# Optimization experiments

Measured on AMD Instinct MI355X. Metric: run time of the kernel, lower is better.

## Reference

```python
import jax, jax.numpy as jnp
import numpy as np

N = 50000
T = 6
E = 800000
F_IN = 64
HID = 64
HEADS = 4
NEG_SLOPE = 0.2
BN_EPS = 1e-5


def _gat_layer(x, src, dst, W, att_src, att_dst, bias, concat):
    # x: [N, Fin]; W: [Fin, H*C]; att_*: [H, C]; src/dst: [E+N] (self loops appended)
    n = x.shape[0]
    H, C = att_src.shape
    xl = (x @ W).reshape(n, H, C)                     # [N, H, C]
    a_src = jnp.sum(xl * att_src[None], axis=-1)      # [N, H]
    a_dst = jnp.sum(xl * att_dst[None], axis=-1)      # [N, H]
    e = jax.nn.leaky_relu(a_src[src] + a_dst[dst], NEG_SLOPE)  # [E', H]
    # segment softmax over destination nodes (every node has a self loop)
    m = jax.ops.segment_max(e, dst, num_segments=n)
    ex = jnp.exp(e - m[dst])
    s = jax.ops.segment_sum(ex, dst, num_segments=n)
    alpha = ex / (s[dst] + 1e-16)                     # [E', H]
    msg = alpha[:, :, None] * xl[src]                 # [E', H, C]
    out = jax.ops.segment_sum(msg, dst, num_segments=n)  # [N, H, C]
    if concat:
        out = out.reshape(n, H * C)
    else:
        out = out.mean(axis=1)
    return out + bias


def _forward(x_seq, edge_index, W1, as1, ad1, b1, W2, as2, ad2, b2,
             cw1, cb1, g1, be1, cw2, cb2, g2, be2, lw1, lb1, lw2, lb2):
    n = x_seq.shape[1]
    self_loop = jnp.arange(n, dtype=edge_index.dtype)
    src = jnp.concatenate([edge_index[0], self_loop])
    dst = jnp.concatenate([edge_index[1], self_loop])

    def per_t(x):
        h = _gat_layer(x, src, dst, W1, as1, ad1, b1, concat=True)
        h = jax.nn.elu(h)
        h = _gat_layer(h, src, dst, W2, as2, ad2, b2, concat=False)
        h = jax.nn.elu(h)
        return h                                      # [N, HID]

    temporal = jax.vmap(per_t)(x_seq)                 # [T, N, HID]
    temporal = jnp.transpose(temporal, (1, 2, 0))     # [N, HID, T]

    def conv_bn_relu(t, cw, cb, g, be):
        y = jax.lax.conv_general_dilated(
            t, cw, window_strides=(1,), padding=[(1, 1)],
            dimension_numbers=('NCH', 'OIH', 'NCH')) + cb[None, :, None]
        # BatchNorm1d in eval mode, running_mean=0, running_var=1
        y = y * (g / jnp.sqrt(1.0 + BN_EPS))[None, :, None] + be[None, :, None]
        return jax.nn.relu(y)

    t = conv_bn_relu(temporal, cw1, cb1, g1, be1)
    t = conv_bn_relu(t, cw2, cb2, g2, be2)
    pooled = t.mean(axis=-1)                          # adaptive avg pool -> [N, HID]
    h = jax.nn.relu(pooled @ lw1 + lb1)
    logits = h @ lw2 + lb2                            # [N, 1]
    return logits


def setup_inputs() -> dict:
    key = jax.random.key(0)
    ks = jax.random.split(key, 20)
    C1 = HID // HEADS  # 16
    s = 0.1
    return {
        'x_seq': jax.random.normal(ks[0], (T, N, F_IN), jnp.float32),
        'edge_index': jax.random.randint(ks[1], (2, E), 0, N, jnp.int32),
        'W1': jax.random.normal(ks[2], (F_IN, HEADS * C1), jnp.float32) * s,
        'as1': jax.random.normal(ks[3], (HEADS, C1), jnp.float32) * s,
        'ad1': jax.random.normal(ks[4], (HEADS, C1), jnp.float32) * s,
        'b1': jnp.zeros((HEADS * C1,), jnp.float32),
        'W2': jax.random.normal(ks[5], (HID, HEADS * HID), jnp.float32) * s,
        'as2': jax.random.normal(ks[6], (HEADS, HID), jnp.float32) * s,
        'ad2': jax.random.normal(ks[7], (HEADS, HID), jnp.float32) * s,
        'b2': jnp.zeros((HID,), jnp.float32),
        'cw1': jax.random.normal(ks[8], (HID, HID, 3), jnp.float32) * s,
        'cb1': jnp.zeros((HID,), jnp.float32),
        'g1': jnp.ones((HID,), jnp.float32),
        'be1': jnp.zeros((HID,), jnp.float32),
        'cw2': jax.random.normal(ks[9], (HID, HID, 3), jnp.float32) * s,
        'cb2': jnp.zeros((HID,), jnp.float32),
        'g2': jnp.ones((HID,), jnp.float32),
        'be2': jnp.zeros((HID,), jnp.float32),
        'lw1': jax.random.normal(ks[10], (HID, HID // 2), jnp.float32) * s,
        'lb1': jnp.zeros((HID // 2,), jnp.float32),
        'lw2': jax.random.normal(ks[11], (HID // 2, 1), jnp.float32) * s,
        'lb2': jnp.zeros((1,), jnp.float32),
    }


def reference(x_seq, edge_index, W1, as1, ad1, b1, W2, as2, ad2, b2,
              cw1, cb1, g1, be1, cw2, cb2, g2, be2, lw1, lb1, lw2, lb2):
    return _forward(x_seq, edge_index, W1, as1, ad1, b1, W2, as2, ad2, b2,
                    cw1, cb1, g1, be1, cw2, cb2, g2, be2, lw1, lb1, lw2, lb2)
```

## Files before the change

kernel.cpp:

```cpp
#include <hip/hip_runtime.h>
#include <math.h>

#define NN 50000
#define EE 800000
#define TT 6

__device__ __forceinline__ float lrelu(float x){ return x > 0.f ? x : 0.2f*x; }
__device__ __forceinline__ float eluf(float x){ return x > 0.f ? x : expm1f(x); }
#define RL(v,i) __uint_as_float(__builtin_amdgcn_readlane(__float_as_uint(v), (i)))

__global__ void k_init_counts(int* __restrict__ c){
  int i = blockIdx.x*256 + threadIdx.x;
  if (i < NN) c[i] = 1;
}

__global__ void k_hist(const int* __restrict__ dst, int* __restrict__ c){
  int i = blockIdx.x*256 + threadIdx.x;
  if (i < EE) atomicAdd(&c[dst[i]], 1);
}

__global__ void k_scanA(const int* __restrict__ cnt, int* __restrict__ excl,
                        int* __restrict__ bsum){
  __shared__ int sh[1024];
  int tid = threadIdx.x;
  int i = blockIdx.x*1024 + tid;
  int v = (i < NN) ? cnt[i] : 0;
  int x = v;
  sh[tid] = x; __syncthreads();
  for (int off = 1; off < 1024; off <<= 1){
    int y = (tid >= off) ? sh[tid - off] : 0;
    __syncthreads();
    x += y; sh[tid] = x; __syncthreads();
  }
  if (i < NN) excl[i] = x - v;
  if (tid == 1023) bsum[blockIdx.x] = x;
}

__global__ void k_scanB(int* __restrict__ bsum, int nb){
  if (threadIdx.x == 0){
    int run = 0;
    for (int b = 0; b < nb; ++b){ int t = bsum[b]; bsum[b] = run; run += t; }
  }
}

__global__ void k_scanC(const int* __restrict__ excl, const int* __restrict__ bsum,
                        int* __restrict__ rowptr, int* __restrict__ cursor){
  int i = blockIdx.x*1024 + threadIdx.x;
  if (i < NN){
    int v = excl[i] + bsum[blockIdx.x];
    rowptr[i] = v; cursor[i] = v;
  }
  if (i == 0) rowptr[NN] = EE + NN;
}

__global__ void k_scatter(const int* __restrict__ ei, int* __restrict__ cursor,
                          int* __restrict__ csr){
  int i = blockIdx.x*256 + threadIdx.x;
  if (i < EE){
    int d = ei[EE + i];
    int p = atomicAdd(&cursor[d], 1);
    csr[p] = ei[i];
  } else if (i < EE + NN){
    int v = i - EE;
    int p = atomicAdd(&cursor[v], 1);
    csr[p] = v;
  }
}

__global__ void k_prep(const float* __restrict__ W1, const float* __restrict__ as1,
                       const float* __restrict__ ad1,
                       const float* __restrict__ W2, const float* __restrict__ as2,
                       const float* __restrict__ ad2,
                       const float* __restrict__ cw1, const float* __restrict__ cw2,
                       float* __restrict__ Was1, float* __restrict__ Wad1,
                       float* __restrict__ Wat2, float* __restrict__ Wb,
                       float4* __restrict__ w1p, float4* __restrict__ w2p){
  int tid = threadIdx.x;
  int k = tid >> 2, h = tid & 3;
  float s1 = 0.f, d1 = 0.f, s2 = 0.f, d2 = 0.f;
  for (int c = 0; c < 16; ++c){
    float w = W1[k*64 + h*16 + c];
    s1 += w * as1[h*16 + c];
    d1 += w * ad1[h*16 + c];
  }
  for (int c = 0; c < 64; ++c){
    float w = W2[k*256 + h*64 + c];
    s2 += w * as2[h*64 + c];
    d2 += w * ad2[h*64 + c];
  }
  Was1[k*4+h] = s1; Wad1[k*4+h] = d1;
  Wat2[k*8 + h] = s2; Wat2[k*8 + 4 + h] = d2;
  for (int idx = tid; idx < 256*64; idx += 256){
    int kf = idx >> 6, c = idx & 63;
    int hh = kf >> 6, kk = kf & 63;
    Wb[idx] = W2[kk*256 + hh*64 + c];
  }
  for (int idx = tid; idx < 64*64; idx += 256){
    int o = idx & 63, i = idx >> 6;
    w1p[idx] = make_float4(cw1[o*192+i*3], cw1[o*192+i*3+1], cw1[o*192+i*3+2], 0.f);
    w2p[idx] = make_float4(cw2[o*192+i*3], cw2[o*192+i*3+1], cw2[o*192+i*3+2], 0.f);
  }
}

__global__ __launch_bounds__(256) void k_gemm_att1(const float* __restrict__ A,
                            const float* __restrict__ W,
                            const float* __restrict__ Was, const float* __restrict__ Wad,
                            float* __restrict__ Xl, float* __restrict__ a_src,
                            float* __restrict__ a_dst){
  __shared__ float At[64][16];
  int tid = threadIdx.x;
  int r0 = blockIdx.x * 16;
  {
    const float4* A4 = (const float4*)(A + (size_t)r0*64);
    float4 v = A4[tid];
    int r = tid >> 4, k4 = (tid & 15) << 2;
    At[k4+0][r] = v.x; At[k4+1][r] = v.y;
    At[k4+2][r] = v.z; At[k4+3][r] = v.w;
  }
  __syncthreads();
  int col = tid & 63;
  int rbase = (tid >> 6) << 2;
  float acc0=0.f, acc1=0.f, acc2=0.f, acc3=0.f;
  for (int k = 0; k < 64; ++k){
    float w = W[k*64 + col];
    float4 a4 = *(const float4*)&At[k][rbase];
    acc0 += a4.x*w; acc1 += a4.y*w; acc2 += a4.z*w; acc3 += a4.w*w;
  }
  Xl[(size_t)(r0+rbase+0)*64 + col] = acc0;
  Xl[(size_t)(r0+rbase+1)*64 + col] = acc1;
  Xl[(size_t)(r0+rbase+2)*64 + col] = acc2;
  Xl[(size_t)(r0+rbase+3)*64 + col] = acc3;
  if (tid < 128){
    int r = tid >> 3, jx = tid & 7;
    int h = jx & 3;
    const float* Wv = (jx < 4) ? Was : Wad;
    float a = 0.f;
    for (int k = 0; k < 64; ++k) a += At[k][r] * Wv[k*4 + h];
    if (jx < 4) a_src[(r0 + r)*4 + h] = a;
    else        a_dst[(r0 + r)*4 + h] = a;
  }
}

__global__ __launch_bounds__(256) void k_att(const float* __restrict__ A,
                                             const float* __restrict__ Wat,
                                             float* __restrict__ a_src,
                                             float* __restrict__ a_dst){
  int lane = threadIdx.x & 63;
  int wid  = threadIdx.x >> 6;
  int q = lane >> 3, j = lane & 7;
  int n = blockIdx.x*32 + wid*8 + q;
  if (n >= NN) return;
  const float* __restrict__ Ar = A + (size_t)n*64;
  float s = 0.f;
#pragma unroll 8
  for (int k = 0; k < 64; ++k) s += Ar[k] * Wat[k*8 + j];
  if (j < 4) a_src[n*4 + j] = s;
  else       a_dst[n*4 + (j-4)] = s;
}

__global__ void k_agg1(const float* __restrict__ xl, const float* __restrict__ a_src,
                       const float* __restrict__ a_dst, const float* __restrict__ b1,
                       const int* __restrict__ rowptr, const int* __restrict__ csr,
                       float* __restrict__ h1){
  int lane = threadIdx.x & 63;
  int wid  = threadIdx.x >> 6;
  int n = blockIdx.x*4 + wid;
  int h = lane >> 4;
  float ad = a_dst[n*4 + h];
  int rs = rowptr[n], re = rowptr[n+1];
  float s = 0.f, acc = 0.f;
  int j = rs;
  for (; j + 4 <= re; j += 4){
    int sn0=csr[j], sn1=csr[j+1], sn2=csr[j+2], sn3=csr[j+3];
    float e0=a_src[sn0*4+h], e1=a_src[sn1*4+h], e2=a_src[sn2*4+h], e3=a_src[sn3*4+h];
    float x0=xl[(size_t)sn0*64+lane], x1=xl[(size_t)sn1*64+lane];
    float x2=xl[(size_t)sn2*64+lane], x3=xl[(size_t)sn3*64+lane];
    float p0=__expf(lrelu(e0+ad)), p1=__expf(lrelu(e1+ad));
    float p2=__expf(lrelu(e2+ad)), p3=__expf(lrelu(e3+ad));
    s += p0; acc += p0*x0;
    s += p1; acc += p1*x1;
    s += p2; acc += p2*x2;
    s += p3; acc += p3*x3;
  }
  for (; j < re; ++j){
    int sn = csr[j];
    float p = __expf(lrelu(a_src[sn*4+h] + ad));
    float x = xl[(size_t)sn*64 + lane];
    s += p; acc += p*x;
  }
  h1[(size_t)n*64 + lane] = eluf(acc/(s + 1e-16f) + b1[lane]);
}

__global__ void k_agg2(const float* __restrict__ h1, const float* __restrict__ a_src,
                       const float* __restrict__ a_dst,
                       const int* __restrict__ rowptr, const int* __restrict__ csr,
                       float* __restrict__ agg){
  int lane = threadIdx.x & 63;
  int wid  = threadIdx.x >> 6;
  int n = blockIdx.x*4 + wid;
  float4 ad = ((const float4*)a_dst)[n];
  int rs = rowptr[n], re = rowptr[n+1];
  float s0=0.f,s1=0.f,s2=0.f,s3=0.f;
  float g0=0.f,g1=0.f,g2=0.f,g3=0.f;
  int j = rs;
  for (; j + 4 <= re; j += 4){
    int sa=csr[j], sb=csr[j+1], sc=csr[j+2], sd=csr[j+3];
    float4 ea = ((const float4*)a_src)[sa];
    float4 eb = ((const float4*)a_src)[sb];
    float4 ec = ((const float4*)a_src)[sc];
    float4 ed = ((const float4*)a_src)[sd];
    float xa = h1[(size_t)sa*64 + lane];
    float xb = h1[(size_t)sb*64 + lane];
    float xc = h1[(size_t)sc*64 + lane];
    float xd = h1[(size_t)sd*64 + lane];
    float pa0=__expf(lrelu(ea.x+ad.x)), pa1=__expf(lrelu(ea.y+ad.y));
    float pa2=__expf(lrelu(ea.z+ad.z)), pa3=__expf(lrelu(ea.w+ad.w));
    float pb0=__expf(lrelu(eb.x+ad.x)), pb1=__expf(lrelu(eb.y+ad.y));
    float pb2=__expf(lrelu(eb.z+ad.z)), pb3=__expf(lrelu(eb.w+ad.w));
    float pc0=__expf(lrelu(ec.x+ad.x)), pc1=__expf(lrelu(ec.y+ad.y));
    float pc2=__expf(lrelu(ec.z+ad.z)), pc3=__expf(lrelu(ec.w+ad.w));
    float pd0=__expf(lrelu(ed.x+ad.x)), pd1=__expf(lrelu(ed.y+ad.y));
    float pd2=__expf(lrelu(ed.z+ad.z)), pd3=__expf(lrelu(ed.w+ad.w));
    s0 += pa0+pb0+pc0+pd0; g0 += pa0*xa + pb0*xb + pc0*xc + pd0*xd;
    s1 += pa1+pb1+pc1+pd1; g1 += pa1*xa + pb1*xb + pc1*xc + pd1*xd;
    s2 += pa2+pb2+pc2+pd2; g2 += pa2*xa + pb2*xb + pc2*xc + pd2*xd;
    s3 += pa3+pb3+pc3+pd3; g3 += pa3*xa + pb3*xb + pc3*xc + pd3*xd;
  }
  for (; j < re; ++j){
    int sn = csr[j];
    float4 ev = ((const float4*)a_src)[sn];
    float x = h1[(size_t)sn*64 + lane];
    float p0=__expf(lrelu(ev.x+ad.x)), p1=__expf(lrelu(ev.y+ad.y));
    float p2=__expf(lrelu(ev.z+ad.z)), p3=__expf(lrelu(ev.w+ad.w));
    s0 += p0; g0 += p0*x;
    s1 += p1; g1 += p1*x;
    s2 += p2; g2 += p2*x;
    s3 += p3; g3 += p3*x;
  }
  size_t base = (size_t)n*256 + lane;
  agg[base      ] = g0/(s0 + 1e-16f);
  agg[base +  64] = g1/(s1 + 1e-16f);
  agg[base + 128] = g2/(s2 + 1e-16f);
  agg[base + 192] = g3/(s3 + 1e-16f);
}

__global__ __launch_bounds__(256) void k_out2(const float* __restrict__ agg,
                                              const float* __restrict__ Wb,
                                              const float* __restrict__ b2,
                                              float* __restrict__ ht){
  int lane = threadIdx.x & 63;
  int wid  = __builtin_amdgcn_readfirstlane(threadIdx.x >> 6);
  int r0 = blockIdx.x*16 + wid*4;
  const float* __restrict__ a0 = agg + (size_t)r0*256;
  float acc0=0.f, acc1=0.f, acc2=0.f, acc3=0.f;
#pragma unroll 4
  for (int k = 0; k < 256; ++k){
    float w = Wb[k*64 + lane];
    acc0 += a0[k      ]*w;
    acc1 += a0[k + 256]*w;
    acc2 += a0[k + 512]*w;
    acc3 += a0[k + 768]*w;
  }
  float bb = b2[lane];
  ht[(size_t)(r0+0)*64 + lane] = eluf(0.25f*acc0 + bb);
  ht[(size_t)(r0+1)*64 + lane] = eluf(0.25f*acc1 + bb);
  ht[(size_t)(r0+2)*64 + lane] = eluf(0.25f*acc2 + bb);
  ht[(size_t)(r0+3)*64 + lane] = eluf(0.25f*acc3 + bb);
}

__global__ __launch_bounds__(256) void k_xpose(const float* __restrict__ htb,
                                               float* __restrict__ Xp){
  int ch = threadIdx.x & 63;
  int q  = threadIdx.x >> 6;
  int n = blockIdx.x*4 + q;
  float r0 = htb[((size_t)0*NN + n)*64 + ch];
  float r1 = htb[((size_t)1*NN + n)*64 + ch];
  float r2 = htb[((size_t)2*NN + n)*64 + ch];
  float r3 = htb[((size_t)3*NN + n)*64 + ch];
  float r4 = htb[((size_t)4*NN + n)*64 + ch];
  float r5 = htb[((size_t)5*NN + n)*64 + ch];
  float* dst = Xp + (size_t)n*384 + ch*6;
  *(float2*)(dst+0) = make_float2(r0,r1);
  *(float2*)(dst+2) = make_float2(r2,r3);
  *(float2*)(dst+4) = make_float2(r4,r5);
}

__global__ __launch_bounds__(256) void k_temporal(
    float* __restrict__ Xp,
    const float4* __restrict__ w1p, const float* __restrict__ cb1,
    const float* __restrict__ g1,   const float* __restrict__ be1,
    const float4* __restrict__ w2p, const float* __restrict__ cb2,
    const float* __restrict__ g2,   const float* __restrict__ be2,
    const float* __restrict__ lw1,  const float* __restrict__ lb1,
    const float* __restrict__ lw2,  const float* __restrict__ lb2,
    float* __restrict__ out){
  int lane = threadIdx.x & 63;
  int wid  = __builtin_amdgcn_readfirstlane(threadIdx.x >> 6);
  int n0 = (blockIdx.x*4 + wid)*4;
  float* xb = Xp + (size_t)n0*384;

  float acc[4][6];
  {
    float c = cb1[lane];
#pragma unroll
    for (int q=0;q<4;++q){
#pragma unroll
      for (int t=0;t<6;++t) acc[q][t]=c;
    }
    for (int i = 0; i < 64; ++i){
      float4 w = w1p[(i<<6) + lane];
      const float* xr = xb + i*6;
#pragma unroll
      for (int q = 0; q < 4; ++q){
        float2 A2 = *(const float2*)(xr + q*384);
        float2 B2 = *(const float2*)(xr + q*384 + 2);
        float2 C2 = *(const float2*)(xr + q*384 + 4);
        acc[q][0] += w.y*A2.x + w.z*A2.y;
        acc[q][1] += w.x*A2.x + w.y*A2.y + w.z*B2.x;
        acc[q][2] += w.x*A2.y + w.y*B2.x + w.z*B2.y;
        acc[q][3] += w.x*B2.x + w.y*B2.y + w.z*C2.x;
        acc[q][4] += w.x*B2.y + w.y*C2.x + w.z*C2.y;
        acc[q][5] += w.x*C2.x + w.y*C2.y;
      }
    }
    float bns = g1[lane]*rsqrtf(1.f + 1e-5f), be = be1[lane];
#pragma unroll
    for (int q=0;q<4;++q){
      float* dp = xb + q*384 + lane*6;
      float r0 = fmaxf(acc[q][0]*bns + be, 0.f);
      float r1 = fmaxf(acc[q][1]*bns + be, 0.f);
      float r2 = fmaxf(acc[q][2]*bns + be, 0.f);
      float r3 = fmaxf(acc[q][3]*bns + be, 0.f);
      float r4 = fmaxf(acc[q][4]*bns + be, 0.f);
      float r5 = fmaxf(acc[q][5]*bns + be, 0.f);
      *(float2*)(dp+0) = make_float2(r0,r1);
      *(float2*)(dp+2) = make_float2(r2,r3);
      *(float2*)(dp+4) = make_float2(r4,r5);
    }
  }
  float p0, p1, p2, p3;
  {
    float c = cb2[lane];
#pragma unroll
    for (int q=0;q<4;++q){
#pragma unroll
      for (int t=0;t<6;++t) acc[q][t]=c;
    }
    for (int i = 0; i < 64; ++i){
      float4 w = w2p[(i<<6) + lane];
      const float* xr = xb + i*6;
#pragma unroll
      for (int q = 0; q < 4; ++q){
        float2 A2 = *(const float2*)(xr + q*384);
        float2 B2 = *(const float2*)(xr + q*384 + 2);
        float2 C2 = *(const float2*)(xr + q*384 + 4);
        acc[q][0] += w.y*A2.x + w.z*A2.y;
        acc[q][1] += w.x*A2.x + w.y*A2.y + w.z*B2.x;
        acc[q][2] += w.x*A2.y + w.y*B2.x + w.z*B2.y;
        acc[q][3] += w.x*B2.x + w.y*B2.y + w.z*C2.x;
        acc[q][4] += w.x*B2.y + w.y*C2.x + w.z*C2.y;
        acc[q][5] += w.x*C2.x + w.y*C2.y;
      }
    }
    float bns = g2[lane]*rsqrtf(1.f + 1e-5f), be = be2[lane];
    float pl[4];
#pragma unroll
    for (int q=0;q<4;++q){
      float s = 0.f;
#pragma unroll
      for (int t=0;t<6;++t) s += fmaxf(acc[q][t]*bns + be, 0.f);
      pl[q] = s*(1.f/6.f);
    }
    p0 = pl[0]; p1 = pl[1]; p2 = pl[2]; p3 = pl[3];
  }
  {
    int j = lane & 31;
    float lb = lb1[j], w2v = lw2[j];
    float h0=0.f, h1v=0.f, h2=0.f, h3=0.f;
    for (int k = 0; k < 64; ++k){
      float lw = lw1[k*32 + j];
      h0  += RL(p0, k)*lw;
      h1v += RL(p1, k)*lw;
      h2  += RL(p2, k)*lw;
      h3  += RL(p3, k)*lw;
    }
    float o0 = fmaxf(h0 +lb, 0.f)*w2v;
    float o1 = fmaxf(h1v+lb, 0.f)*w2v;
    float o2 = fmaxf(h2 +lb, 0.f)*w2v;
    float o3 = fmaxf(h3 +lb, 0.f)*w2v;
#pragma unroll
    for (int off = 16; off >= 1; off >>= 1){
      o0 += __shfl_xor(o0, off);
      o1 += __shfl_xor(o1, off);
      o2 += __shfl_xor(o2, off);
      o3 += __shfl_xor(o3, off);
    }
    if (lane == 0){
      float b = lb2[0];
      out[n0+0] = o0 + b;
      out[n0+1] = o1 + b;
      out[n0+2] = o2 + b;
      out[n0+3] = o3 + b;
    }
  }
}

extern "C" void kernel_launch(void* const* d_in, const int* in_sizes, int n_in,
                              void* d_out, int out_size, void* d_ws, size_t ws_size,
                              hipStream_t stream) {
  const float* x_seq = (const float*)d_in[0];
  const int*   ei    = (const int*)  d_in[1];
  const float* W1  = (const float*)d_in[2];
  const float* as1 = (const float*)d_in[3];
  const float* ad1 = (const float*)d_in[4];
  const float* b1  = (const float*)d_in[5];
  const float* W2  = (const float*)d_in[6];
  const float* as2 = (const float*)d_in[7];
  const float* ad2 = (const float*)d_in[8];
  const float* b2  = (const float*)d_in[9];
  const float* cw1 = (const float*)d_in[10];
  const float* cb1 = (const float*)d_in[11];
  const float* g1  = (const float*)d_in[12];
  const float* be1 = (const float*)d_in[13];
  const float* cw2 = (const float*)d_in[14];
  const float* cb2 = (const float*)d_in[15];
  const float* g2  = (const float*)d_in[16];
  const float* be2 = (const float*)d_in[17];
  const float* lw1 = (const float*)d_in[18];
  const float* lb1 = (const float*)d_in[19];
  const float* lw2 = (const float*)d_in[20];
  const float* lb2 = (const float*)d_in[21];
  float* out = (float*)d_out;

  char* wp = (char*)d_ws;
  auto alloc = [&](size_t bytes) -> char* {
    char* p = wp; wp += (bytes + 255) & ~(size_t)255; return p;
  };
  float* htb  = (float*)alloc((size_t)TT*NN*64*sizeof(float));
  float* Was1 = (float*)alloc(256*sizeof(float));
  float* Wad1 = (float*)alloc(256*sizeof(float));
  float* Wat2 = (float*)alloc(64*8*sizeof(float));
  float* Wb   = (float*)alloc(256*64*sizeof(float));
  float4* w1p = (float4*)alloc(64*64*sizeof(float4));
  float4* w2p = (float4*)alloc(64*64*sizeof(float4));
  char* scratch0 = wp;
  int*   counts = (int*)  alloc(NN*sizeof(int));
  int*   excl   = (int*)  alloc(NN*sizeof(int));
  int*   bsum   = (int*)  alloc(64*sizeof(int));
  int*   rowptr = (int*)  alloc((NN+1)*sizeof(int));
  int*   cursor = (int*)  alloc(NN*sizeof(int));
  int*   csr    = (int*)  alloc((size_t)(EE+NN)*sizeof(int));
  float* a_src  = (float*)alloc((size_t)NN*4*sizeof(float));
  float* a_dst  = (float*)alloc((size_t)NN*4*sizeof(float));
  float* h1     = (float*)alloc((size_t)NN*64*sizeof(float));
  float* agg    = (float*)alloc((size_t)NN*256*sizeof(float));
  float* xl1    = agg;
  float* Xp     = (float*)scratch0;

  const int NBSCAN = (NN + 1023)/1024;
  k_init_counts<<<(NN+255)/256, 256, 0, stream>>>(counts);
  k_hist<<<(EE+255)/256, 256, 0, stream>>>(ei + EE, counts);
  k_scanA<<<NBSCAN, 1024, 0, stream>>>(counts, excl, bsum);
  k_scanB<<<1, 64, 0, stream>>>(bsum, NBSCAN);
  k_scanC<<<NBSCAN, 1024, 0, stream>>>(excl, bsum, rowptr, cursor);
  k_scatter<<<(EE+NN+255)/256, 256, 0, stream>>>(ei, cursor, csr);
  k_prep<<<1, 256, 0, stream>>>(W1, as1, ad1, W2, as2, ad2, cw1, cw2,
                                Was1, Wad1, Wat2, Wb, w1p, w2p);

  for (int t = 0; t < TT; ++t){
    const float* xt = x_seq + (size_t)t*NN*64;
    k_gemm_att1<<<NN/16, 256, 0, stream>>>(xt, W1, Was1, Wad1, xl1, a_src, a_dst);
    k_agg1<<<NN/4, 256, 0, stream>>>(xl1, a_src, a_dst, b1, rowptr, csr, h1);
    k_att<<<(NN+31)/32, 256, 0, stream>>>(h1, Wat2, a_src, a_dst);
    k_agg2<<<NN/4, 256, 0, stream>>>(h1, a_src, a_dst, rowptr, csr, agg);
    k_out2<<<NN/16, 256, 0, stream>>>(agg, Wb, b2, htb + (size_t)t*NN*64);
  }
  k_xpose<<<NN/4, 256, 0, stream>>>(htb, Xp);
  k_temporal<<<NN/16, 256, 0, stream>>>(Xp, w1p, cb1, g1, be1, w2p, cb2, g2, be2,
                                        lw1, lb1, lw2, lb2, out);
}
```

Before: 1.623 ms.

## Fuse layer-2 attention into agg1, tile out2 via LDS, restructure temporal conv

The layer-2 attention projection (the separate k_att kernel) is folded into k_agg1 through a wave shuffle reduction, which removes one launch and one re-read of h1 per timestep. k_out2 now stages the aggregated rows transposed in shared memory and reads them from LDS instead of issuing scalar global loads. The temporal stage moves to a channel-major, zero-padded layout with one node per lane, spread across two kernels (transpose, then fused conv1+conv2+pool+MLP), so weights become wave-uniform and activation loads are coalesced. The cost is an extra global round trip through the C1 buffer and heavy workspace aliasing, which brings buffer-reuse risk.

After: 1.432 ms. 1.13x faster.

```diff
diff --git a/kernel.cpp b/kernel.cpp
--- a/kernel.cpp
+++ b/kernel.cpp
@@ -7,7 +7,6 @@
 
 __device__ __forceinline__ float lrelu(float x){ return x > 0.f ? x : 0.2f*x; }
 __device__ __forceinline__ float eluf(float x){ return x > 0.f ? x : expm1f(x); }
-#define RL(v,i) __uint_as_float(__builtin_amdgcn_readlane(__float_as_uint(v), (i)))
 
 __global__ void k_init_counts(int* __restrict__ c){
   int i = blockIdx.x*256 + threadIdx.x;
@@ -72,9 +71,11 @@
                        const float* __restrict__ W2, const float* __restrict__ as2,
                        const float* __restrict__ ad2,
                        const float* __restrict__ cw1, const float* __restrict__ cw2,
+                       const float* __restrict__ lw1,
                        float* __restrict__ Was1, float* __restrict__ Wad1,
                        float* __restrict__ Wat2, float* __restrict__ Wb,
-                       float4* __restrict__ w1p, float4* __restrict__ w2p){
+                       float4* __restrict__ wq1, float4* __restrict__ wq2,
+                       float* __restrict__ lw1t){
   int tid = threadIdx.x;
   int k = tid >> 2, h = tid & 3;
   float s1 = 0.f, d1 = 0.f, s2 = 0.f, d2 = 0.f;
@@ -96,9 +97,13 @@
     Wb[idx] = W2[kk*256 + hh*64 + c];
   }
   for (int idx = tid; idx < 64*64; idx += 256){
-    int o = idx & 63, i = idx >> 6;
-    w1p[idx] = make_float4(cw1[o*192+i*3], cw1[o*192+i*3+1], cw1[o*192+i*3+2], 0.f);
-    w2p[idx] = make_float4(cw2[o*192+i*3], cw2[o*192+i*3+1], cw2[o*192+i*3+2], 0.f);
+    int o = idx >> 6, i = idx & 63;
+    wq1[idx] = make_float4(cw1[o*192+i*3], cw1[o*192+i*3+1], cw1[o*192+i*3+2], 0.f);
+    wq2[idx] = make_float4(cw2[o*192+i*3], cw2[o*192+i*3+1], cw2[o*192+i*3+2], 0.f);
+  }
+  for (int idx = tid; idx < 32*64; idx += 256){
+    int j = idx >> 6, kk = idx & 63;
+    lw1t[idx] = lw1[kk*32 + j];
   }
 }
 
@@ -141,27 +146,12 @@
   }
 }
 
-__global__ __launch_bounds__(256) void k_att(const float* __restrict__ A,
-                                             const float* __restrict__ Wat,
-                                             float* __restrict__ a_src,
-                                             float* __restrict__ a_dst){
-  int lane = threadIdx.x & 63;
-  int wid  = threadIdx.x >> 6;
-  int q = lane >> 3, j = lane & 7;
-  int n = blockIdx.x*32 + wid*8 + q;
-  if (n >= NN) return;
-  const float* __restrict__ Ar = A + (size_t)n*64;
-  float s = 0.f;
-#pragma unroll 8
-  for (int k = 0; k < 64; ++k) s += Ar[k] * Wat[k*8 + j];
-  if (j < 4) a_src[n*4 + j] = s;
-  else       a_dst[n*4 + (j-4)] = s;
-}
-
 __global__ void k_agg1(const float* __restrict__ xl, const float* __restrict__ a_src,
                        const float* __restrict__ a_dst, const float* __restrict__ b1,
+                       const float* __restrict__ Wat2,
                        const int* __restrict__ rowptr, const int* __restrict__ csr,
-                       float* __restrict__ h1){
+                       float* __restrict__ h1,
+                       float* __restrict__ a_src2, float* __restrict__ a_dst2){
   int lane = threadIdx.x & 63;
   int wid  = threadIdx.x >> 6;
   int n = blockIdx.x*4 + wid;
@@ -188,7 +178,22 @@
     float x = xl[(size_t)sn*64 + lane];
     s += p; acc += p*x;
   }
-  h1[(size_t)n*64 + lane] = eluf(acc/(s + 1e-16f) + b1[lane]);
+  float hv = eluf(acc/(s + 1e-16f) + b1[lane]);
+  h1[(size_t)n*64 + lane] = hv;
+  float4 wA = ((const float4*)Wat2)[lane*2];
+  float4 wB = ((const float4*)Wat2)[lane*2 + 1];
+  float p[8];
+  p[0]=hv*wA.x; p[1]=hv*wA.y; p[2]=hv*wA.z; p[3]=hv*wA.w;
+  p[4]=hv*wB.x; p[5]=hv*wB.y; p[6]=hv*wB.z; p[7]=hv*wB.w;
+#pragma unroll
+  for (int off = 32; off >= 1; off >>= 1){
+#pragma unroll
+    for (int q = 0; q < 8; ++q) p[q] += __shfl_xor(p[q], off);
+  }
+  if (lane == 0){
+    ((float4*)a_src2)[n] = make_float4(p[0],p[1],p[2],p[3]);
+    ((float4*)a_dst2)[n] = make_float4(p[4],p[5],p[6],p[7]);
+  }
 }
 
 __global__ void k_agg2(const float* __restrict__ h1, const float* __restrict__ a_src,
@@ -248,161 +253,177 @@
                                               const float* __restrict__ Wb,
                                               const float* __restrict__ b2,
                                               float* __restrict__ ht){
-  int lane = threadIdx.x & 63;
-  int wid  = __builtin_amdgcn_readfirstlane(threadIdx.x >> 6);
-  int r0 = blockIdx.x*16 + wid*4;
-  const float* __restrict__ a0 = agg + (size_t)r0*256;
+  __shared__ float AtF[256*20];
+  int tid = threadIdx.x;
+  int r0 = blockIdx.x * 16;
+  const float4* A4 = (const float4*)(agg + (size_t)r0*256);
+#pragma unroll
+  for (int jj = 0; jj < 4; ++jj){
+    int m = tid + 256*jj;
+    float4 v = A4[m];
+    int row = m >> 6, k0 = (m & 63) << 2;
+    AtF[(k0+0)*20 + row] = v.x;
+    AtF[(k0+1)*20 + row] = v.y;
+    AtF[(k0+2)*20 + row] = v.z;
+    AtF[(k0+3)*20 + row] = v.w;
+  }
+  __syncthreads();
+  int col = tid & 63;
+  int rbase = (tid >> 6) << 2;
   float acc0=0.f, acc1=0.f, acc2=0.f, acc3=0.f;
-#pragma unroll 4
   for (int k = 0; k < 256; ++k){
-    float w = Wb[k*64 + lane];
-    acc0 += a0[k      ]*w;
-    acc1 += a0[k + 256]*w;
-    acc2 += a0[k + 512]*w;
-    acc3 += a0[k + 768]*w;
-  }
-  float bb = b2[lane];
-  ht[(size_t)(r0+0)*64 + lane] = eluf(0.25f*acc0 + bb);
-  ht[(size_t)(r0+1)*64 + lane] = eluf(0.25f*acc1 + bb);
-  ht[(size_t)(r0+2)*64 + lane] = eluf(0.25f*acc2 + bb);
-  ht[(size_t)(r0+3)*64 + lane] = eluf(0.25f*acc3 + bb);
-}
-
-__global__ __launch_bounds__(256) void k_xpose(const float* __restrict__ htb,
-                                               float* __restrict__ Xp){
-  int ch = threadIdx.x & 63;
-  int q  = threadIdx.x >> 6;
-  int n = blockIdx.x*4 + q;
-  float r0 = htb[((size_t)0*NN + n)*64 + ch];
-  float r1 = htb[((size_t)1*NN + n)*64 + ch];
-  float r2 = htb[((size_t)2*NN + n)*64 + ch];
-  float r3 = htb[((size_t)3*NN + n)*64 + ch];
-  float r4 = htb[((size_t)4*NN + n)*64 + ch];
-  float r5 = htb[((size_t)5*NN + n)*64 + ch];
-  float* dst = Xp + (size_t)n*384 + ch*6;
-  *(float2*)(dst+0) = make_float2(r0,r1);
-  *(float2*)(dst+2) = make_float2(r2,r3);
-  *(float2*)(dst+4) = make_float2(r4,r5);
-}
-
-__global__ __launch_bounds__(256) void k_temporal(
-    float* __restrict__ Xp,
-    const float4* __restrict__ w1p, const float* __restrict__ cb1,
+    float w = Wb[(size_t)k*64 + col];
+    float4 a4 = *(const float4*)&AtF[k*20 + rbase];
+    acc0 += a4.x*w; acc1 += a4.y*w; acc2 += a4.z*w; acc3 += a4.w*w;
+  }
+  float bb = b2[col];
+  ht[(size_t)(r0+rbase+0)*64 + col] = eluf(0.25f*acc0 + bb);
+  ht[(size_t)(r0+rbase+1)*64 + col] = eluf(0.25f*acc1 + bb);
+  ht[(size_t)(r0+rbase+2)*64 + col] = eluf(0.25f*acc2 + bb);
+  ht[(size_t)(r0+rbase+3)*64 + col] = eluf(0.25f*acc3 + bb);
+}
+
+__global__ __launch_bounds__(256) void k_xposeQ(const float* __restrict__ htb,
+                                                float* __restrict__ Xq){
+  __shared__ float T[64][65];
+  int tid = threadIdx.x;
+  int q = tid >> 6, lane = tid & 63;
+  int n0 = blockIdx.x * 64;
+  int nw = n0 + lane;
+  bool ok = (nw < NN);
+  for (int jj = 0; jj < 16; ++jj){
+    int ch = q*16 + jj;
+    if (ok){
+      Xq[((size_t)ch*8 + 0)*NN + nw] = 0.f;
+      Xq[((size_t)ch*8 + 7)*NN + nw] = 0.f;
+    }
+  }
+  for (int t = 0; t < 6; ++t){
+    for (int jj = 0; jj < 16; ++jj){
+      int nn = q*16 + jj;
+      int nsrc = n0 + nn; if (nsrc >= NN) nsrc = NN-1;
+      T[nn][lane] = htb[((size_t)t*NN + nsrc)*64 + lane];
+    }
+    __syncthreads();
+    if (ok){
+      for (int jj = 0; jj < 16; ++jj){
+        int ch = q*16 + jj;
+        Xq[((size_t)ch*8 + t + 1)*NN + nw] = T[lane][ch];
+      }
+    }
+    __syncthreads();
+  }
+}
+
+__global__ __launch_bounds__(256) void k_convQ(
+    const float* __restrict__ Xq, float* __restrict__ C1,
+    const float4* __restrict__ wq1, const float* __restrict__ cb1,
     const float* __restrict__ g1,   const float* __restrict__ be1,
-    const float4* __restrict__ w2p, const float* __restrict__ cb2,
+    const float4* __restrict__ wq2, const float* __restrict__ cb2,
     const float* __restrict__ g2,   const float* __restrict__ be2,
-    const float* __restrict__ lw1,  const float* __restrict__ lb1,
+    const float* __restrict__ lw1t, const float* __restrict__ lb1,
     const float* __restrict__ lw2,  const float* __restrict__ lb2,
     float* __restrict__ out){
+  __shared__ float pool_lds[64][65];
+  __shared__ float outp[4][64];
   int lane = threadIdx.x & 63;
-  int wid  = __builtin_amdgcn_readfirstlane(threadIdx.x >> 6);
-  int n0 = (blockIdx.x*4 + wid)*4;
-  float* xb = Xp + (size_t)n0*384;
-
-  float acc[4][6];
+  int w = __builtin_amdgcn_readfirstlane(threadIdx.x >> 6);
+  int n0 = blockIdx.x * 64;
+  int n = n0 + lane;
+  int nc = (n < NN) ? n : (NN-1);
+  bool ok = (n < NN);
+
+#pragma unroll
+  for (int oc = 0; oc < 2; ++oc){
+    int ob = w*16 + oc*8;
+    float acc[8][6];
+#pragma unroll
+    for (int o = 0; o < 8; ++o){
+      float c = cb1[ob+o];
+#pragma unroll
+      for (int t = 0; t < 6; ++t) acc[o][t] = c;
+    }
+    for (int i = 0; i < 64; ++i){
+      const float* xp = Xq + (size_t)i*8*NN + nc;
+      float x0 = xp[0*NN], x1 = xp[1*NN], x2 = xp[2*NN], x3 = xp[3*NN];
+      float x4 = xp[4*NN], x5 = xp[5*NN], x6 = xp[6*NN], x7 = xp[7*NN];
+#pragma unroll
+      for (int o = 0; o < 8; ++o){
+        float4 wv = wq1[(ob+o)*64 + i];
+        acc[o][0] += wv.x*x0 + wv.y*x1 + wv.z*x2;
+        acc[o][1] += wv.x*x1 + wv.y*x2 + wv.z*x3;
+        acc[o][2] += wv.x*x2 + wv.y*x3 + wv.z*x4;
+        acc[o][3] += wv.x*x3 + wv.y*x4 + wv.z*x5;
+        acc[o][4] += wv.x*x4 + wv.y*x5 + wv.z*x6;
+        acc[o][5] += wv.x*x5 + wv.y*x6 + wv.z*x7;
+      }
+    }
+    if (ok){
+#pragma unroll
+      for (int o = 0; o < 8; ++o){
+        float bns = g1[ob+o]*rsqrtf(1.f + 1e-5f), be = be1[ob+o];
+        float* cp = C1 + (size_t)(ob+o)*8*NN + n;
+        cp[0*NN] = 0.f; cp[7*NN] = 0.f;
+#pragma unroll
+        for (int t = 0; t < 6; ++t) cp[(t+1)*NN] = fmaxf(acc[o][t]*bns + be, 0.f);
+      }
+    }
+  }
+  __syncthreads();
+#pragma unroll
+  for (int oc = 0; oc < 2; ++oc){
+    int ob = w*16 + oc*8;
+    float acc[8][6];
+#pragma unroll
+    for (int o = 0; o < 8; ++o){
+      float c = cb2[ob+o];
+#pragma unroll
+      for (int t = 0; t < 6; ++t) acc[o][t] = c;
+    }
+    for (int i = 0; i < 64; ++i){
+      const float* xp = C1 + (size_t)i*8*NN + nc;
+      float x0 = xp[0*NN], x1 = xp[1*NN], x2 = xp[2*NN], x3 = xp[3*NN];
+      float x4 = xp[4*NN], x5 = xp[5*NN], x6 = xp[6*NN], x7 = xp[7*NN];
+#pragma unroll
+      for (int o = 0; o < 8; ++o){
+        float4 wv = wq2[(ob+o)*64 + i];
+        acc[o][0] += wv.x*x0 + wv.y*x1 + wv.z*x2;
+        acc[o][1] += wv.x*x1 + wv.y*x2 + wv.z*x3;
+        acc[o][2] += wv.x*x2 + wv.y*x3 + wv.z*x4;
+        acc[o][3] += wv.x*x3 + wv.y*x4 + wv.z*x5;
+        acc[o][4] += wv.x*x4 + wv.y*x5 + wv.z*x6;
+        acc[o][5] += wv.x*x5 + wv.y*x6 + wv.z*x7;
+      }
+    }
+#pragma unroll
+    for (int o = 0; o < 8; ++o){
+      float bns = g2[ob+o]*rsqrtf(1.f + 1e-5f), be = be2[ob+o];
+      float pooled = 0.f;
+#pragma unroll
+      for (int t = 0; t < 6; ++t) pooled += fmaxf(acc[o][t]*bns + be, 0.f);
+      pool_lds[ob+o][lane] = pooled*(1.f/6.f);
+    }
+  }
+  __syncthreads();
   {
-    float c = cb1[lane];
-#pragma unroll
-    for (int q=0;q<4;++q){
-#pragma unroll
-      for (int t=0;t<6;++t) acc[q][t]=c;
-    }
-    for (int i = 0; i < 64; ++i){
-      float4 w = w1p[(i<<6) + lane];
-      const float* xr = xb + i*6;
-#pragma unroll
-      for (int q = 0; q < 4; ++q){
-        float2 A2 = *(const float2*)(xr + q*384);
-        float2 B2 = *(const float2*)(xr + q*384 + 2);
-        float2 C2 = *(const float2*)(xr + q*384 + 4);
-        acc[q][0] += w.y*A2.x + w.z*A2.y;
-        acc[q][1] += w.x*A2.x + w.y*A2.y + w.z*B2.x;
-        acc[q][2] += w.x*A2.y + w.y*B2.x + w.z*B2.y;
-        acc[q][3] += w.x*B2.x + w.y*B2.y + w.z*C2.x;
-        acc[q][4] += w.x*B2.y + w.y*C2.x + w.z*C2.y;
-        acc[q][5] += w.x*C2.x + w.y*C2.y;
-      }
-    }
-    float bns = g1[lane]*rsqrtf(1.f + 1e-5f), be = be1[lane];
-#pragma unroll
-    for (int q=0;q<4;++q){
-      float* dp = xb + q*384 + lane*6;
-      float r0 = fmaxf(acc[q][0]*bns + be, 0.f);
-      float r1 = fmaxf(acc[q][1]*bns + be, 0.f);
-      float r2 = fmaxf(acc[q][2]*bns + be, 0.f);
-      float r3 = fmaxf(acc[q][3]*bns + be, 0.f);
-      float r4 = fmaxf(acc[q][4]*bns + be, 0.f);
-      float r5 = fmaxf(acc[q][5]*bns + be, 0.f);
-      *(float2*)(dp+0) = make_float2(r0,r1);
-      *(float2*)(dp+2) = make_float2(r2,r3);
-      *(float2*)(dp+4) = make_float2(r4,r5);
-    }
-  }
-  float p0, p1, p2, p3;
-  {
-    float c = cb2[lane];
-#pragma unroll
-    for (int q=0;q<4;++q){
-#pragma unroll
-      for (int t=0;t<6;++t) acc[q][t]=c;
-    }
-    for (int i = 0; i < 64; ++i){
-      float4 w = w2p[(i<<6) + lane];
-      const float* xr = xb + i*6;
-#pragma unroll
-      for (int q = 0; q < 4; ++q){
-        float2 A2 = *(const float2*)(xr + q*384);
-        float2 B2 = *(const float2*)(xr + q*384 + 2);
-        float2 C2 = *(const float2*)(xr + q*384 + 4);
-        acc[q][0] += w.y*A2.x + w.z*A2.y;
-        acc[q][1] += w.x*A2.x + w.y*A2.y + w.z*B2.x;
-        acc[q][2] += w.x*A2.y + w.y*B2.x + w.z*B2.y;
-        acc[q][3] += w.x*B2.x + w.y*B2.y + w.z*C2.x;
-        acc[q][4] += w.x*B2.y + w.y*C2.x + w.z*C2.y;
-        acc[q][5] += w.x*C2.x + w.y*C2.y;
-      }
-    }
-    float bns = g2[lane]*rsqrtf(1.f + 1e-5f), be = be2[lane];
-    float pl[4];
-#pragma unroll
-    for (int q=0;q<4;++q){
-      float s = 0.f;
-#pragma unroll
-      for (int t=0;t<6;++t) s += fmaxf(acc[q][t]*bns + be, 0.f);
-      pl[q] = s*(1.f/6.f);
-    }
-    p0 = pl[0]; p1 = pl[1]; p2 = pl[2]; p3 = pl[3];
-  }
-  {
-    int j = lane & 31;
-    float lb = lb1[j], w2v = lw2[j];
-    float h0=0.f, h1v=0.f, h2=0.f, h3=0.f;
+    float hacc[8];
+#pragma unroll
+    for (int jj = 0; jj < 8; ++jj) hacc[jj] = 0.f;
     for (int k = 0; k < 64; ++k){
-      float lw = lw1[k*32 + j];
-      h0  += RL(p0, k)*lw;
-      h1v += RL(p1, k)*lw;
-      h2  += RL(p2, k)*lw;
-      h3  += RL(p3, k)*lw;
-    }
-    float o0 = fmaxf(h0 +lb, 0.f)*w2v;
-    float o1 = fmaxf(h1v+lb, 0.f)*w2v;
-    float o2 = fmaxf(h2 +lb, 0.f)*w2v;
-    float o3 = fmaxf(h3 +lb, 0.f)*w2v;
-#pragma unroll
-    for (int off = 16; off >= 1; off >>= 1){
-      o0 += __shfl_xor(o0, off);
-      o1 += __shfl_xor(o1, off);
-      o2 += __shfl_xor(o2, off);
-      o3 += __shfl_xor(o3, off);
-    }
-    if (lane == 0){
-      float b = lb2[0];
-      out[n0+0] = o0 + b;
-      out[n0+1] = o1 + b;
-      out[n0+2] = o2 + b;
-      out[n0+3] = o3 + b;
-    }
-  }
+      float pk = pool_lds[k][lane];
+#pragma unroll
+      for (int jj = 0; jj < 8; ++jj)
+        hacc[jj] += pk * lw1t[(w*8+jj)*64 + k];
+    }
+    float po = 0.f;
+#pragma unroll
+    for (int jj = 0; jj < 8; ++jj)
+      po += fmaxf(hacc[jj] + lb1[w*8+jj], 0.f) * lw2[w*8+jj];
+    outp[w][lane] = po;
+  }
+  __syncthreads();
+  if (w == 0 && ok)
+    out[n] = outp[0][lane] + outp[1][lane] + outp[2][lane] + outp[3][lane] + lb2[0];
 }
 
 extern "C" void kernel_launch(void* const* d_in, const int* in_sizes, int n_in,
@@ -432,30 +453,41 @@
   const float* lb2 = (const float*)d_in[21];
   float* out = (float*)d_out;
 
+  const size_t QSZ = (size_t)64*8*NN*sizeof(float);
   char* wp = (char*)d_ws;
   auto alloc = [&](size_t bytes) -> char* {
     char* p = wp; wp += (bytes + 255) & ~(size_t)255; return p;
   };
-  float* htb  = (float*)alloc((size_t)TT*NN*64*sizeof(float));
+  char* region1 = alloc(QSZ);
   float* Was1 = (float*)alloc(256*sizeof(float));
   float* Wad1 = (float*)alloc(256*sizeof(float));
   float* Wat2 = (float*)alloc(64*8*sizeof(float));
   float* Wb   = (float*)alloc(256*64*sizeof(float));
-  float4* w1p = (float4*)alloc(64*64*sizeof(float4));
-  float4* w2p = (float4*)alloc(64*64*sizeof(float4));
-  char* scratch0 = wp;
-  int*   counts = (int*)  alloc(NN*sizeof(int));
-  int*   excl   = (int*)  alloc(NN*sizeof(int));
-  int*   bsum   = (int*)  alloc(64*sizeof(int));
-  int*   rowptr = (int*)  alloc((NN+1)*sizeof(int));
-  int*   cursor = (int*)  alloc(NN*sizeof(int));
-  int*   csr    = (int*)  alloc((size_t)(EE+NN)*sizeof(int));
-  float* a_src  = (float*)alloc((size_t)NN*4*sizeof(float));
-  float* a_dst  = (float*)alloc((size_t)NN*4*sizeof(float));
-  float* h1     = (float*)alloc((size_t)NN*64*sizeof(float));
-  float* agg    = (float*)alloc((size_t)NN*256*sizeof(float));
+  float4* wq1 = (float4*)alloc(64*64*sizeof(float4));
+  float4* wq2 = (float4*)alloc(64*64*sizeof(float4));
+  float* lw1t = (float*)alloc(32*64*sizeof(float));
+  char* region2 = alloc(QSZ);
+
+  char* sp = region1;
+  auto salloc = [&](size_t bytes) -> char* {
+    char* p = sp; sp += (bytes + 255) & ~(size_t)255; return p;
+  };
+  int*   counts = (int*)  salloc(NN*sizeof(int));
+  int*   excl   = (int*)  salloc(NN*sizeof(int));
+  int*   bsum   = (int*)  salloc(64*sizeof(int));
+  int*   rowptr = (int*)  salloc((NN+1)*sizeof(int));
+  int*   cursor = (int*)  salloc(NN*sizeof(int));
+  int*   csr    = (int*)  salloc((size_t)(EE+NN)*sizeof(int));
+  float* a_src1 = (float*)salloc((size_t)NN*4*sizeof(float));
+  float* a_dst1 = (float*)salloc((size_t)NN*4*sizeof(float));
+  float* a_src2 = (float*)salloc((size_t)NN*4*sizeof(float));
+  float* a_dst2 = (float*)salloc((size_t)NN*4*sizeof(float));
+  float* h1     = (float*)salloc((size_t)NN*64*sizeof(float));
+  float* agg    = (float*)salloc((size_t)NN*256*sizeof(float));
   float* xl1    = agg;
-  float* Xp     = (float*)scratch0;
+  float* Xq     = (float*)region1;
+  float* htb    = (float*)region2;
+  float* C1     = (float*)region2;
 
   const int NBSCAN = (NN + 1023)/1024;
   k_init_counts<<<(NN+255)/256, 256, 0, stream>>>(counts);
@@ -464,18 +496,19 @@
   k_scanB<<<1, 64, 0, stream>>>(bsum, NBSCAN);
   k_scanC<<<NBSCAN, 1024, 0, stream>>>(excl, bsum, rowptr, cursor);
   k_scatter<<<(EE+NN+255)/256, 256, 0, stream>>>(ei, cursor, csr);
-  k_prep<<<1, 256, 0, stream>>>(W1, as1, ad1, W2, as2, ad2, cw1, cw2,
-                                Was1, Wad1, Wat2, Wb, w1p, w2p);
+  k_prep<<<1, 256, 0, stream>>>(W1, as1, ad1, W2, as2, ad2, cw1, cw2, lw1,
+                                Was1, Wad1, Wat2, Wb, wq1, wq2, lw1t);
 
   for (int t = 0; t < TT; ++t){
     const float* xt = x_seq + (size_t)t*NN*64;
-    k_gemm_att1<<<NN/16, 256, 0, stream>>>(xt, W1, Was1, Wad1, xl1, a_src, a_dst);
-    k_agg1<<<NN/4, 256, 0, stream>>>(xl1, a_src, a_dst, b1, rowptr, csr, h1);
-    k_att<<<(NN+31)/32, 256, 0, stream>>>(h1, Wat2, a_src, a_dst);
-    k_agg2<<<NN/4, 256, 0, stream>>>(h1, a_src, a_dst, rowptr, csr, agg);
+    k_gemm_att1<<<NN/16, 256, 0, stream>>>(xt, W1, Was1, Wad1, xl1, a_src1, a_dst1);
+    k_agg1<<<NN/4, 256, 0, stream>>>(xl1, a_src1, a_dst1, b1, Wat2, rowptr, csr,
+                                     h1, a_src2, a_dst2);
+    k_agg2<<<NN/4, 256, 0, stream>>>(h1, a_src2, a_dst2, rowptr, csr, agg);
     k_out2<<<NN/16, 256, 0, stream>>>(agg, Wb, b2, htb + (size_t)t*NN*64);
   }
-  k_xpose<<<NN/4, 256, 0, stream>>>(htb, Xp);
-  k_temporal<<<NN/16, 256, 0, stream>>>(Xp, w1p, cb1, g1, be1, w2p, cb2, g2, be2,
-                                        lw1, lb1, lw2, lb2, out);
-}
+  const int NB64 = (NN + 63)/64;
+  k_xposeQ<<<NB64, 256, 0, stream>>>(htb, Xq);
+  k_convQ<<<NB64, 256, 0, stream>>>(Xq, C1, wq1, cb1, g1, be1, wq2, cb2, g2, be2,
+                                    lw1t, lb1, lw2, lb2, out);
+}
```
